# Kernel tuning notes

Hardware: AMD Instinct MI355X
Metric: run time of the kernel (lower is better)

The kernel has to match this reference:

```python
import jax, jax.numpy as jnp
import numpy as np

B, T, HW, N, HID, K, OUT = 8, 64, 64, 64, 64, 2, 1
DT = 0.1


def setup_inputs() -> dict:
    key = jax.random.key(0)
    ks = jax.random.split(key, 16)
    nrm = lambda k, shape, s: jax.random.normal(k, shape, jnp.float32) * s
    return {
        "frames": jax.random.uniform(ks[0], (B, T, HW, HW, 3), jnp.float32),
        "adjacency": jax.random.uniform(ks[1], (B, T, N, N), jnp.float32) / N,
        "hidden0": jnp.zeros((B, N, HID), jnp.float32),
        "Wc1": nrm(ks[2], (32, 3, 3, 3), 0.3), "bc1": jnp.zeros(32, jnp.float32),
        "Wc2": nrm(ks[3], (64, 32, 3, 3), 0.08), "bc2": jnp.zeros(64, jnp.float32),
        "Wc3": nrm(ks[4], (128, 64, 3, 3), 0.06), "bc3": jnp.zeros(128, jnp.float32),
        "We": nrm(ks[5], (128, HID), 0.09), "be": jnp.zeros(HID, jnp.float32),
        "Wh": nrm(ks[6], (K + 1, HID, HID), 0.12),
        "Wx": nrm(ks[7], (K + 1, HID, HID), 0.12),
        "bg": jnp.zeros(HID, jnp.float32),
        "tau": jnp.ones(HID, jnp.float32),
        "Ap": nrm(ks[8], (HID,), 1.0),
        "Wd1": nrm(ks[9], (HID, 128), 0.12), "bd1": jnp.zeros(128, jnp.float32),
        "Wd2": nrm(ks[10], (128, 64), 0.09), "bd2": jnp.zeros(64, jnp.float32),
        "Wd3": nrm(ks[11], (64, OUT), 0.12), "bd3": jnp.zeros(OUT, jnp.float32),
    }


def _conv_relu(x, w, b, stride):
    # torch Conv2d(k=3, stride=2, padding=1) == explicit padding (1,1)
    y = jax.lax.conv_general_dilated(
        x, w, (stride, stride), [(1, 1), (1, 1)],
        dimension_numbers=("NCHW", "OIHW", "NCHW"))
    return jax.nn.relu(y + b[None, :, None, None])


def _forward(frames, adjacency, hidden0, Wc1, bc1, Wc2, bc2, Wc3, bc3,
             We, be, Wh, Wx, bg, tau, Ap, Wd1, bd1, Wd2, bd2, Wd3, bd3):
    Bn, Tn, Hh, Ww, C = frames.shape
    # faithful to torch .view(-1, C, H, W): raw memory reinterpretation
    x = frames.reshape(Bn * Tn, C, Hh, Ww)
    x = _conv_relu(x, Wc1, bc1, 2)   # [BT,32,32,32]
    x = _conv_relu(x, Wc2, bc2, 2)   # [BT,64,16,16]
    x = _conv_relu(x, Wc3, bc3, 2)   # [BT,128,8,8]; AdaptiveAvgPool2d((8,8)) is identity here
    feats = x.reshape(Bn, Tn, 128, 8, 8).transpose(0, 1, 3, 4, 2).reshape(Bn, Tn, 64, 128)
    node = feats @ We + be           # [B,T,N,HID]

    Kp = Wh.shape[0] - 1
    eye = jnp.eye(adjacency.shape[-1], dtype=frames.dtype)

    def step(h, inputs):
        xt, At = inputs              # [B,N,HID], [B,N,N]
        powers = [jnp.broadcast_to(eye, At.shape)]
        p = At
        for _ in range(Kp):          # static K-loop -> [I, A, ..., A^K]
            powers.append(p)
            p = jnp.matmul(p, At)
        S = jnp.stack(powers)        # [K+1,B,N,N]
        z = jnp.einsum("bnd,kde->kbne", h, Wh) + jnp.einsum("bnd,kde->kbne", xt, Wx)
        gc = jnp.einsum("kbnm,kbme->bne", S, z) + bg
        f = jnp.tanh(gc)
        h_next = h + DT * (-(1.0 / tau + f) * h + f * Ap)  # liquid time-constant Euler step
        m = h_next.mean(axis=1)      # [B,HID]
        d = jax.nn.relu(m @ Wd1 + bd1)
        d = jax.nn.relu(d @ Wd2 + bd2)
        c = d @ Wd3 + bd3            # [B,OUT]
        return h_next, c

    xs = (node.transpose(1, 0, 2, 3), adjacency.transpose(1, 0, 2, 3))
    final_h, controls = jax.lax.scan(step, hidden0, xs)
    controls = controls.transpose(1, 0, 2)  # [B,T,OUT]
    return controls, final_h


def reference(frames, adjacency, hidden0, Wc1, bc1, Wc2, bc2, Wc3, bc3,
              We, be, Wh, Wx, bg, tau, Ap, Wd1, bd1, Wd2, bd2, Wd3, bd3):
    return _forward(frames, adjacency, hidden0, Wc1, bc1, Wc2, bc2, Wc3, bc3,
                    We, be, Wh, Wx, bg, tau, Ap, Wd1, bd1, Wd2, bd2, Wd3, bd3)
```

## Files before the change

### kernel.cpp

```cpp
#include <hip/hip_runtime.h>
#include <hip/hip_bf16.h>

#define SH 68
#define DT_C 0.1f

typedef short bfrag __attribute__((ext_vector_type(8)));
typedef _Float16 hfrag __attribute__((ext_vector_type(8)));
typedef float f32x4 __attribute__((ext_vector_type(4)));

union FU { bfrag v; unsigned short s[8]; uint4 q; };
union HU { hfrag v; unsigned short s[8]; uint4 q; };

__device__ __forceinline__ unsigned short bf16_rn(float x) {
  union { float f; unsigned u; } v; v.f = x;
  unsigned r = v.u + 0x7fffu + ((v.u >> 16) & 1u);
  return (unsigned short)(r >> 16);
}
__device__ __forceinline__ float bf16_tof(unsigned short h) {
  union { unsigned u; float f; } v; v.u = ((unsigned)h) << 16; return v.f;
}
__device__ __forceinline__ unsigned short bfu(float x) {
  union { __hip_bfloat16 b; unsigned short u; } cv;
  cv.b = __float2bfloat16(x);
  return cv.u;
}
__device__ __forceinline__ float tanh_f(float x) {
  return 1.0f - 2.0f / (__expf(2.0f * x) + 1.0f);
}
__device__ __forceinline__ void h16split(float v, unsigned short& hu, unsigned short& lu) {
  union { _Float16 h; unsigned short u; } a, b;
  a.h = (_Float16)v;
  b.h = (_Float16)(v - (float)a.h);
  hu = a.u; lu = b.u;
}
__device__ __forceinline__ unsigned short h16hi(float v) {
  union { _Float16 h; unsigned short u; } a; a.h = (_Float16)v; return a.u;
}

__device__ __forceinline__ void mm16(const float* __restrict__ A,
                                     const float* __restrict__ B, int sb,
                                     float acc[4][4], int n0, int e0) {
  #pragma unroll 4
  for (int k4 = 0; k4 < 16; ++k4) {
    float4 av0 = *(const float4*)(A + (n0+0)*SH + k4*4);
    float4 av1 = *(const float4*)(A + (n0+1)*SH + k4*4);
    float4 av2 = *(const float4*)(A + (n0+2)*SH + k4*4);
    float4 av3 = *(const float4*)(A + (n0+3)*SH + k4*4);
    const float a0j[4] = {av0.x, av0.y, av0.z, av0.w};
    const float a1j[4] = {av1.x, av1.y, av1.z, av1.w};
    const float a2j[4] = {av2.x, av2.y, av2.z, av2.w};
    const float a3j[4] = {av3.x, av3.y, av3.z, av3.w};
    #pragma unroll
    for (int j = 0; j < 4; ++j) {
      const float4 bv = *(const float4*)(B + (k4*4+j)*sb + e0);
      acc[0][0]+=a0j[j]*bv.x; acc[0][1]+=a0j[j]*bv.y; acc[0][2]+=a0j[j]*bv.z; acc[0][3]+=a0j[j]*bv.w;
      acc[1][0]+=a1j[j]*bv.x; acc[1][1]+=a1j[j]*bv.y; acc[1][2]+=a1j[j]*bv.z; acc[1][3]+=a1j[j]*bv.w;
      acc[2][0]+=a2j[j]*bv.x; acc[2][1]+=a2j[j]*bv.y; acc[2][2]+=a2j[j]*bv.z; acc[2][3]+=a2j[j]*bv.w;
      acc[3][0]+=a3j[j]*bv.x; acc[3][1]+=a3j[j]*bv.y; acc[3][2]+=a3j[j]*bv.z; acc[3][3]+=a3j[j]*bv.w;
    }
  }
}

__global__ __launch_bounds__(256) void wprep_k(const float* __restrict__ Wc2,
                                               const float* __restrict__ Wc3,
                                               const float* __restrict__ Wh,
                                               const float* __restrict__ We,
                                               unsigned short* __restrict__ W2h,
                                               unsigned short* __restrict__ W2l,
                                               unsigned short* __restrict__ W3h,
                                               unsigned short* __restrict__ W3l,
                                               unsigned short* __restrict__ WTh,
                                               unsigned short* __restrict__ WTl,
                                               unsigned short* __restrict__ WeTh,
                                               unsigned short* __restrict__ WeTl) {
  int i = blockIdx.x * 256 + threadIdx.x;
  if (i < 18432) {
    int oc = i / 288, rem = i % 288, pos = rem >> 5, ic = rem & 31;
    float v = Wc2[oc*288 + ic*9 + pos];
    h16split(v, W2h[i], W2l[i]);
  } else if (i < 18432 + 73728) {
    int j = i - 18432;
    int oc = j / 576, rem = j % 576, pos = rem >> 6, ic = rem & 63;
    float v = Wc3[oc*576 + ic*9 + pos];
    h16split(v, W3h[j], W3l[j]);
  } else if (i < 18432 + 73728 + 12288) {
    int j = i - 92160;
    int k3 = j >> 12, rem = j & 4095, din = rem >> 6, dout = rem & 63;
    float v = Wh[j];
    unsigned short hi = bf16_rn(v);
    WTh[k3*4096 + dout*64 + din] = hi;
    WTl[k3*4096 + dout*64 + din] = bf16_rn(v - bf16_tof(hi));
  } else if (i < 18432 + 73728 + 12288 + 8192) {
    int j = i - 104448;
    int e = j >> 7, oc = j & 127;
    float v = We[oc*64 + e];
    h16split(v, WeTh[j], WeTl[j]);
  }
}

__global__ __launch_bounds__(256) void conv1_k(const float* __restrict__ frames,
                                               const float* __restrict__ W,
                                               const float* __restrict__ bias,
                                               unsigned short* __restrict__ c1h) {
  __shared__ __align__(16) float sIn[12288];
  int bt = blockIdx.x, tid = threadIdx.x;
  const float4* src = (const float4*)(frames + (size_t)bt * 12288);
  for (int i = tid; i < 3072; i += 256) ((float4*)sIn)[i] = src[i];
  __syncthreads();
  for (int p = tid; p < 1024; p += 256) {
    int ho = p >> 5, wo = p & 31, hi0 = ho*2-1, wi0 = wo*2-1;
    int obase = (((ho*2 + (wo&1))*16 + (wo>>1)))*8;
    for (int ocb = 0; ocb < 4; ++ocb) {
      float acc[8];
      #pragma unroll
      for (int j = 0; j < 8; ++j) acc[j] = bias[ocb*8+j];
      for (int ic = 0; ic < 3; ++ic) {
        float win[9];
        #pragma unroll
        for (int kh = 0; kh < 3; ++kh) {
          int hi = hi0 + kh;
          #pragma unroll
          for (int kw = 0; kw < 3; ++kw) {
            int wi = wi0 + kw;
            win[kh*3+kw] = (hi>=0 && hi<64 && wi>=0 && wi<64) ? sIn[ic*4096 + hi*64 + wi] : 0.f;
          }
        }
        #pragma unroll
        for (int j = 0; j < 8; ++j) {
          const float* wp = W + (size_t)(ocb*8+j)*27 + ic*9;
          #pragma unroll
          for (int k = 0; k < 9; ++k) acc[j] += win[k] * wp[k];
        }
      }
      ushort hh[8];
      #pragma unroll
      for (int j = 0; j < 8; ++j) hh[j] = h16hi(fmaxf(acc[j], 0.f));
      *(uint4*)&c1h[(size_t)bt*32768 + ocb*8192 + obase] = *(uint4*)hh;
    }
  }
}

#define MFMAH(a, bb, cc) __builtin_amdgcn_mfma_f32_16x16x32_f16((a), (bb), (cc), 0, 0, 0)

__global__ __launch_bounds__(256) void conv2m_k(const unsigned short* __restrict__ c1h,
                                                const unsigned short* __restrict__ W2h,
                                                const unsigned short* __restrict__ W2l,
                                                const float* __restrict__ bias,
                                                unsigned short* __restrict__ c2h) {
  __shared__ __align__(16) unsigned short sH[32768];
  int bt = blockIdx.x, tid = threadIdx.x;
  {
    const uint4* gh = (const uint4*)(c1h + (size_t)bt*32768);
    for (int i = tid; i < 4096; i += 256) ((uint4*)sH)[i] = gh[i];
  }
  __syncthreads();
  int lane = tid & 63, w = tid >> 6, g = lane >> 4, c = lane & 15;
  f32x4 acc[4][4] = {};
  const uint4 z4 = make_uint4(0,0,0,0);
  #pragma unroll
  for (int pos = 0; pos < 9; ++pos) {
    const int kh = pos / 3, kw = pos % 3;
    HU Ah[4];
    #pragma unroll
    for (int m = 0; m < 4; ++m) {
      int pix = w*64 + m*16 + c;
      int ho = pix >> 4, wo = pix & 15;
      int hi = 2*ho - 1 + kh, wi = 2*wo - 1 + kw;
      bool ok = (hi >= 0) & (wi >= 0);
      int hic = ok ? hi : 0, wic = ok ? wi : 0;
      int a = (((g*32 + hic)*2 + (wic & 1))*16 + (wic >> 1))*8;
      uint4 vh = *(const uint4*)&sH[a];
      Ah[m].q = ok ? vh : z4;
    }
    HU Bh[4], Bl[4];
    #pragma unroll
    for (int n = 0; n < 4; ++n) {
      int off = (n*16 + c)*288 + pos*32 + g*8;
      Bh[n].q = *(const uint4*)(W2h + off);
      Bl[n].q = *(const uint4*)(W2l + off);
    }
    #pragma unroll
    for (int m = 0; m < 4; ++m)
      #pragma unroll
      for (int n = 0; n < 4; ++n) {
        acc[m][n] = MFMAH(Ah[m].v, Bh[n].v, acc[m][n]);
        acc[m][n] = MFMAH(Ah[m].v, Bl[n].v, acc[m][n]);
      }
  }
  #pragma unroll
  for (int n = 0; n < 4; ++n) {
    int oc = n*16 + c;
    float bv = bias[oc];
    int ks3 = oc >> 3, il = oc & 7;
    #pragma unroll
    for (int m = 0; m < 4; ++m) {
      #pragma unroll
      for (int r = 0; r < 4; ++r) {
        int pix = w*64 + m*16 + 4*g + r;
        int ho = pix >> 4, wo = pix & 15;
        float v = fmaxf(acc[m][n][r] + bv, 0.f);
        size_t dst = (size_t)bt*16384 + ((((ks3*16 + ho)*2 + (wo&1))*8 + (wo>>1)))*8 + il;
        c2h[dst] = h16hi(v);
      }
    }
  }
}

__global__ __launch_bounds__(256) void conv3e_k(const unsigned short* __restrict__ c2h,
                                                const unsigned short* __restrict__ W3h,
                                                const unsigned short* __restrict__ W3l,
                                                const float* __restrict__ bias,
                                                const unsigned short* __restrict__ WeTh,
                                                const unsigned short* __restrict__ WeTl,
                                                const float* __restrict__ be,
                                                float* __restrict__ node) {
  __shared__ __align__(16) unsigned short sH[16384];
  __shared__ __align__(16) unsigned short sF[64*136];
  int bt = blockIdx.x, tid = threadIdx.x;
  {
    const uint4* gh = (const uint4*)(c2h + (size_t)bt*16384);
    for (int i = tid; i < 2048; i += 256) ((uint4*)sH)[i] = gh[i];
  }
  __syncthreads();
  int lane = tid & 63, w = tid >> 6, g = lane >> 4, c = lane & 15;
  f32x4 acc[8] = {};
  const uint4 z4 = make_uint4(0,0,0,0);
  int pix = w*16 + c;
  int ho = pix >> 3, wo = pix & 7;
  #pragma unroll
  for (int pos = 0; pos < 9; ++pos) {
    const int kh = pos / 3, kw = pos % 3;
    int hi = 2*ho - 1 + kh, wi = 2*wo - 1 + kw;
    bool ok = (hi >= 0) & (wi >= 0);
    int hic = ok ? hi : 0, wic = ok ? wi : 0;
    #pragma unroll
    for (int ih = 0; ih < 2; ++ih) {
      int icg = ih*4 + g;
      int a = ((((icg*16 + hic)*2 + (wic & 1))*8 + (wic >> 1)))*8;
      HU Ah;
      uint4 vh = *(const uint4*)&sH[a];
      Ah.q = ok ? vh : z4;
      #pragma unroll
      for (int n = 0; n < 8; ++n) {
        int off = (n*16 + c)*576 + pos*64 + ih*32 + g*8;
        HU Bh, Bl;
        Bh.q = *(const uint4*)(W3h + off);
        Bl.q = *(const uint4*)(W3l + off);
        acc[n] = MFMAH(Ah.v, Bh.v, acc[n]);
        acc[n] = MFMAH(Ah.v, Bl.v, acc[n]);
      }
    }
  }
  #pragma unroll
  for (int n = 0; n < 8; ++n) {
    int oc = n*16 + c;
    float bv = bias[oc];
    #pragma unroll
    for (int r = 0; r < 4; ++r) {
      int po = w*16 + 4*g + r;
      sF[po*136 + oc] = h16hi(fmaxf(acc[n][r] + bv, 0.f));
    }
  }
  __syncthreads();
  f32x4 eacc[4] = {{0.f,0.f,0.f,0.f},{0.f,0.f,0.f,0.f},{0.f,0.f,0.f,0.f},{0.f,0.f,0.f,0.f}};
  #pragma unroll
  for (int kt = 0; kt < 4; ++kt) {
    HU Af;
    Af.q = *(const uint4*)&sF[(w*16 + c)*136 + kt*32 + g*8];
    #pragma unroll
    for (int n = 0; n < 4; ++n) {
      int off = (n*16 + c)*128 + kt*32 + g*8;
      HU Bh, Bl;
      Bh.q = *(const uint4*)(WeTh + off);
      Bl.q = *(const uint4*)(WeTl + off);
      eacc[n] = MFMAH(Af.v, Bh.v, eacc[n]);
      eacc[n] = MFMAH(Af.v, Bl.v, eacc[n]);
    }
  }
  #pragma unroll
  for (int n = 0; n < 4; ++n) {
    int e = n*16 + c;
    float bev = be[e];
    #pragma unroll
    for (int r = 0; r < 4; ++r) {
      int po = w*16 + 4*g + r;
      node[(size_t)bt*4096 + po*64 + e] = eacc[n][r] + bev;
    }
  }
}

__global__ __launch_bounds__(256) void prep_k(const float* __restrict__ adj,
                                              const float* __restrict__ node,
                                              const float* __restrict__ Wx,
                                              unsigned short* __restrict__ Abf,
                                              unsigned short* __restrict__ A2bf,
                                              float* __restrict__ gxg) {
  __shared__ __align__(16) float sA[64*SH], sA2[64*SH], sN[64*SH], sZ[64*SH];
  int bt = blockIdx.x, tid = threadIdx.x;
  {
    const float4* a4 = (const float4*)(adj + (size_t)bt * 4096);
    const float4* n4 = (const float4*)(node + (size_t)bt * 4096);
    for (int i = tid; i < 1024; i += 256) {
      int r = i >> 4, c = (i & 15) * 4;
      *(float4*)&sA[r*SH+c] = a4[i];
      *(float4*)&sN[r*SH+c] = n4[i];
    }
  }
  __syncthreads();
  int lane = tid & 63, w = tid >> 6, nsub = lane >> 4, eb = lane & 15;
  int n0 = w*16 + nsub*4, e0 = eb*4;
  float4* gxout = (float4*)(gxg + (size_t)bt * 4096);
  for (int i = tid; i < 1024; i += 256) {
    int r = i >> 4, c0 = (i & 15) * 4;
    ushort4 o;
    o.x = bf16_rn(sA[r*SH+c0+0]); o.y = bf16_rn(sA[r*SH+c0+1]);
    o.z = bf16_rn(sA[r*SH+c0+2]); o.w = bf16_rn(sA[r*SH+c0+3]);
    *(ushort4*)&Abf[(size_t)bt*4096 + r*64 + c0] = o;
  }
  {
    float a2t[4][4] = {};
    mm16(sA, sA, SH, a2t, n0, e0);
    #pragma unroll
    for (int jj = 0; jj < 4; ++jj) {
      *(float4*)&sA2[(n0+jj)*SH+e0] = make_float4(a2t[jj][0], a2t[jj][1], a2t[jj][2], a2t[jj][3]);
      ushort4 o;
      o.x = bf16_rn(a2t[jj][0]); o.y = bf16_rn(a2t[jj][1]);
      o.z = bf16_rn(a2t[jj][2]); o.w = bf16_rn(a2t[jj][3]);
      *(ushort4*)&A2bf[(size_t)bt*4096 + (n0+jj)*64 + e0] = o;
    }
  }
  {
    float t[4][4] = {};
    mm16(sN, Wx + 4096, 64, t, n0, e0);
    #pragma unroll
    for (int jj = 0; jj < 4; ++jj)
      *(float4*)&sZ[(n0+jj)*SH+e0] = make_float4(t[jj][0], t[jj][1], t[jj][2], t[jj][3]);
  }
  __syncthreads();
  float gx[4][4] = {};
  mm16(sA, sZ, SH, gx, n0, e0);
  __syncthreads();
  {
    float t[4][4] = {};
    mm16(sN, Wx + 8192, 64, t, n0, e0);
    #pragma unroll
    for (int jj = 0; jj < 4; ++jj)
      *(float4*)&sZ[(n0+jj)*SH+e0] = make_float4(t[jj][0], t[jj][1], t[jj][2], t[jj][3]);
  }
  __syncthreads();
  mm16(sA2, sZ, SH, gx, n0, e0);
  mm16(sN, Wx, 64, gx, n0, e0);
  #pragma unroll
  for (int jj = 0; jj < 4; ++jj)
    gxout[(n0+jj)*16 + eb] = make_float4(gx[jj][0], gx[jj][1], gx[jj][2], gx[jj][3]);
}

#define MFMA(a, bb, cc) __builtin_amdgcn_mfma_f32_16x16x32_bf16((a), (bb), (cc), 0, 0, 0)

__global__ __launch_bounds__(1024, 4) void seq2_k(
    const unsigned short* __restrict__ Abf, const unsigned short* __restrict__ A2bf,
    const float* __restrict__ gxg, const float* __restrict__ h0,
    const unsigned short* __restrict__ WTh, const unsigned short* __restrict__ WTl,
    const float* __restrict__ bg, const float* __restrict__ tau, const float* __restrict__ Apv,
    float* __restrict__ mout, float* __restrict__ out) {
  __shared__ unsigned short sHh[64*72];
  __shared__ unsigned short sA[2][64*72], sA2[2][64*72];
  __shared__ unsigned short sZ1[64*72], sZ2[64*72];
  __shared__ float sPart[64*17];
  int b = blockIdx.x, tid = threadIdx.x;
  int lane = tid & 63, w = tid >> 6, g = lane >> 4, c = lane & 15;
  int mt = w & 3, nt = w >> 2;
  int e = nt*16 + c;
  int mrow = mt*16 + 4*g;
  float itau = 1.f/tau[e], apv = Apv[e], bgv = bg[e];
  FU wf[3][2][2];
  #pragma unroll
  for (int k3 = 0; k3 < 3; ++k3)
    #pragma unroll
    for (int kt = 0; kt < 2; ++kt) {
      int off = k3*4096 + e*64 + kt*32 + 8*g;
      wf[k3][kt][0].q = *(const uint4*)(WTh + off);
      wf[k3][kt][1].q = *(const uint4*)(WTl + off);
    }
  float hm[4];
  #pragma unroll
  for (int r = 0; r < 4; ++r) hm[r] = h0[(size_t)b*4096 + (mrow+r)*64 + e];
  #pragma unroll
  for (int r = 0; r < 4; ++r) sHh[(mrow+r)*72 + e] = bfu(hm[r]);
  {
    int row = tid >> 4, k0 = (tid & 15) * 4;
    *(uint2*)&sA[0][row*72 + k0]  = *(const uint2*)(Abf  + (size_t)b*64*4096 + tid*4);
    *(uint2*)&sA2[0][row*72 + k0] = *(const uint2*)(A2bf + (size_t)b*64*4096 + tid*4);
  }
  __syncthreads();
  #pragma unroll 1
  for (int t = 0; t < 64; ++t) {
    int cur = t & 1;
    size_t bt = (size_t)b*64 + t;
    int tn = (t < 63) ? t + 1 : t;
    uint2 pa  = *(const uint2*)(Abf  + ((size_t)b*64 + tn)*4096 + tid*4);
    uint2 pa2 = *(const uint2*)(A2bf + ((size_t)b*64 + tn)*4096 + tid*4);
    float gxv[4];
    {
      const float* gp = gxg + bt*4096;
      #pragma unroll
      for (int r = 0; r < 4; ++r) gxv[r] = gp[(mrow+r)*64 + e];
    }
    FU ha[2];
    #pragma unroll
    for (int kt = 0; kt < 2; ++kt)
      ha[kt].q = *(const uint4*)&sHh[(mt*16 + c)*72 + kt*32 + 8*g];
    f32x4 a1 = {0.f,0.f,0.f,0.f}, a2 = {0.f,0.f,0.f,0.f};
    #pragma unroll
    for (int kt = 0; kt < 2; ++kt) {
      a1 = MFMA(ha[kt].v, wf[1][kt][0].v, a1);
      a1 = MFMA(ha[kt].v, wf[1][kt][1].v, a1);
      a2 = MFMA(ha[kt].v, wf[2][kt][0].v, a2);
      a2 = MFMA(ha[kt].v, wf[2][kt][1].v, a2);
    }
    {
      ushort4 o1, o2;
      o1.x = bfu(a1[0]); o1.y = bfu(a1[1]); o1.z = bfu(a1[2]); o1.w = bfu(a1[3]);
      o2.x = bfu(a2[0]); o2.y = bfu(a2[1]); o2.z = bfu(a2[2]); o2.w = bfu(a2[3]);
      *(ushort4*)&sZ1[e*72 + mrow] = o1;
      *(ushort4*)&sZ2[e*72 + mrow] = o2;
    }
    __syncthreads();
    f32x4 acc = {0.f,0.f,0.f,0.f};
    #pragma unroll
    for (int kt = 0; kt < 2; ++kt) {
      FU aA, aA2, z1f, z2f;
      int ao = (mt*16 + c)*72 + kt*32 + 8*g;
      aA.q  = *(const uint4*)&sA[cur][ao];
      aA2.q = *(const uint4*)&sA2[cur][ao];
      z1f.q = *(const uint4*)&sZ1[e*72 + kt*32 + 8*g];
      z2f.q = *(const uint4*)&sZ2[e*72 + kt*32 + 8*g];
      acc = MFMA(ha[kt].v, wf[0][kt][0].v, acc);
      acc = MFMA(ha[kt].v, wf[0][kt][1].v, acc);
      acc = MFMA(aA.v,  z1f.v, acc);
      acc = MFMA(aA2.v, z2f.v, acc);
    }
    float ps = 0.f;
    #pragma unroll
    for (int r = 0; r < 4; ++r) {
      float gc = acc[r] + gxv[r] + bgv;
      float f = tanh_f(gc);
      float hn = hm[r] + DT_C * (-(itau + f) * hm[r] + f * apv);
      hm[r] = hn;
      ps += hn;
      sHh[(mrow+r)*72 + e] = bfu(hn);
    }
    sPart[e*17 + mt*4 + g] = ps;
    {
      int row = tid >> 4, k0 = (tid & 15) * 4;
      *(uint2*)&sA[cur^1][row*72 + k0]  = pa;
      *(uint2*)&sA2[cur^1][row*72 + k0] = pa2;
    }
    __syncthreads();
    if (lane < 4) {
      int ee = w*4 + lane;
      float s = 0.f;
      #pragma unroll
      for (int j = 0; j < 16; ++j) s += sPart[ee*17 + j];
      mout[bt*64 + ee] = s * (1.0f / 64.0f);
    }
  }
  #pragma unroll
  for (int r = 0; r < 4; ++r)
    out[512 + (size_t)b*4096 + (mrow+r)*64 + e] = hm[r];
}

__global__ __launch_bounds__(128) void dec_k(const float* __restrict__ mout,
                                             const float* __restrict__ Wd1, const float* __restrict__ bd1,
                                             const float* __restrict__ Wd2, const float* __restrict__ bd2,
                                             const float* __restrict__ Wd3, const float* __restrict__ bd3,
                                             float* __restrict__ out) {
  __shared__ float sm[64], sd1[128], sd2[64];
  int bt = blockIdx.x, tid = threadIdx.x;
  if (tid < 64) sm[tid] = mout[(size_t)bt*64 + tid];
  __syncthreads();
  {
    float a = bd1[tid];
    #pragma unroll 8
    for (int e = 0; e < 64; ++e) a += sm[e] * Wd1[e*128 + tid];
    sd1[tid] = fmaxf(a, 0.f);
  }
  __syncthreads();
  if (tid < 64) {
    float a = bd2[tid];
    #pragma unroll 8
    for (int i = 0; i < 128; ++i) a += sd1[i] * Wd2[i*64 + tid];
    sd2[tid] = fmaxf(a, 0.f);
  }
  __syncthreads();
  if (tid < 64) {
    float p = sd2[tid] * Wd3[tid];
    #pragma unroll
    for (int off = 32; off > 0; off >>= 1) p += __shfl_down(p, off, 64);
    if (tid == 0) out[bt] = p + bd3[0];
  }
}

extern "C" void kernel_launch(void* const* d_in, const int* in_sizes, int n_in,
                              void* d_out, int out_size, void* d_ws, size_t ws_size,
                              hipStream_t stream) {
  const float* frames = (const float*)d_in[0];
  const float* adj    = (const float*)d_in[1];
  const float* h0     = (const float*)d_in[2];
  const float* Wc1 = (const float*)d_in[3];  const float* bc1 = (const float*)d_in[4];
  const float* Wc2 = (const float*)d_in[5];  const float* bc2 = (const float*)d_in[6];
  const float* Wc3 = (const float*)d_in[7];  const float* bc3 = (const float*)d_in[8];
  const float* We  = (const float*)d_in[9];  const float* be  = (const float*)d_in[10];
  const float* Wh  = (const float*)d_in[11]; const float* Wx  = (const float*)d_in[12];
  const float* bg  = (const float*)d_in[13]; const float* tau = (const float*)d_in[14];
  const float* Ap  = (const float*)d_in[15];
  const float* Wd1 = (const float*)d_in[16]; const float* bd1 = (const float*)d_in[17];
  const float* Wd2 = (const float*)d_in[18]; const float* bd2 = (const float*)d_in[19];
  const float* Wd3 = (const float*)d_in[20]; const float* bd3 = (const float*)d_in[21];

  float* ws = (float*)d_ws;
  unsigned short* c1h = (unsigned short*)(ws);
  unsigned short* c2h = (unsigned short*)(ws + 16777216);
  unsigned short* W2h = (unsigned short*)(ws + 20971520);
  unsigned short* W2l = (unsigned short*)(ws + 20980736);
  unsigned short* W3h = (unsigned short*)(ws + 20989952);
  unsigned short* W3l = (unsigned short*)(ws + 21026816);
  unsigned short* WTh = (unsigned short*)(ws + 21063680);
  unsigned short* WTl = (unsigned short*)(ws + 21069824);
  unsigned short* WeTh = (unsigned short*)(ws + 21075968);
  unsigned short* WeTl = (unsigned short*)(ws + 21080064);
  float* node = ws + 4194304;
  float* gx   = ws + 6291456;
  unsigned short* Abf  = (unsigned short*)(ws + 8388608);
  unsigned short* A2bf = (unsigned short*)(ws + 9437184);
  float* mo   = ws + 10485760;
  float* out  = (float*)d_out;

  wprep_k <<<440, 256, 0, stream>>>(Wc2, Wc3, Wh, We, W2h, W2l, W3h, W3l, WTh, WTl, WeTh, WeTl);
  conv1_k <<<512, 256, 0, stream>>>(frames, Wc1, bc1, c1h);
  conv2m_k<<<512, 256, 0, stream>>>(c1h, W2h, W2l, bc2, c2h);
  conv3e_k<<<512, 256, 0, stream>>>(c2h, W3h, W3l, bc3, WeTh, WeTl, be, node);
  prep_k  <<<512, 256, 0, stream>>>(adj, node, Wx, Abf, A2bf, gx);
  seq2_k  <<<8,  1024, 0, stream>>>(Abf, A2bf, gx, h0, WTh, WTl, bg, tau, Ap, mo, out);
  dec_k   <<<512, 128, 0, stream>>>(mo, Wd1, bd1, Wd2, bd2, Wd3, bd3, out);
}
```

Measured before the change: 302.2 us.

## Fuse conv1, conv2, conv3, embedding and graph prep into one per-frame kernel

```diff
diff --git a/kernel.cpp b/kernel.cpp
--- a/kernel.cpp
+++ b/kernel.cpp
@@ -37,26 +37,18 @@
   union { _Float16 h; unsigned short u; } a; a.h = (_Float16)v; return a.u;
 }
 
-__device__ __forceinline__ void mm16(const float* __restrict__ A,
-                                     const float* __restrict__ B, int sb,
-                                     float acc[4][4], int n0, int e0) {
+__device__ __forceinline__ void mm1x4(const float* __restrict__ A,
+                                      const float* __restrict__ B, int sb,
+                                      float acc[4], int n, int e0) {
   #pragma unroll 4
   for (int k4 = 0; k4 < 16; ++k4) {
-    float4 av0 = *(const float4*)(A + (n0+0)*SH + k4*4);
-    float4 av1 = *(const float4*)(A + (n0+1)*SH + k4*4);
-    float4 av2 = *(const float4*)(A + (n0+2)*SH + k4*4);
-    float4 av3 = *(const float4*)(A + (n0+3)*SH + k4*4);
-    const float a0j[4] = {av0.x, av0.y, av0.z, av0.w};
-    const float a1j[4] = {av1.x, av1.y, av1.z, av1.w};
-    const float a2j[4] = {av2.x, av2.y, av2.z, av2.w};
-    const float a3j[4] = {av3.x, av3.y, av3.z, av3.w};
+    float4 av = *(const float4*)(A + n*SH + k4*4);
+    const float aj[4] = {av.x, av.y, av.z, av.w};
     #pragma unroll
     for (int j = 0; j < 4; ++j) {
       const float4 bv = *(const float4*)(B + (k4*4+j)*sb + e0);
-      acc[0][0]+=a0j[j]*bv.x; acc[0][1]+=a0j[j]*bv.y; acc[0][2]+=a0j[j]*bv.z; acc[0][3]+=a0j[j]*bv.w;
-      acc[1][0]+=a1j[j]*bv.x; acc[1][1]+=a1j[j]*bv.y; acc[1][2]+=a1j[j]*bv.z; acc[1][3]+=a1j[j]*bv.w;
-      acc[2][0]+=a2j[j]*bv.x; acc[2][1]+=a2j[j]*bv.y; acc[2][2]+=a2j[j]*bv.z; acc[2][3]+=a2j[j]*bv.w;
-      acc[3][0]+=a3j[j]*bv.x; acc[3][1]+=a3j[j]*bv.y; acc[3][2]+=a3j[j]*bv.z; acc[3][3]+=a3j[j]*bv.w;
+      acc[0] += aj[j]*bv.x; acc[1] += aj[j]*bv.y;
+      acc[2] += aj[j]*bv.z; acc[3] += aj[j]*bv.w;
     }
   }
 }
@@ -98,261 +90,206 @@
   }
 }
 
-__global__ __launch_bounds__(256) void conv1_k(const float* __restrict__ frames,
-                                               const float* __restrict__ W,
-                                               const float* __restrict__ bias,
-                                               unsigned short* __restrict__ c1h) {
-  __shared__ __align__(16) float sIn[12288];
+#define MFMAH(a, bb, cc) __builtin_amdgcn_mfma_f32_16x16x32_f16((a), (bb), (cc), 0, 0, 0)
+
+__global__ __launch_bounds__(1024, 4) void mega_k(
+    const float* __restrict__ frames, const float* __restrict__ Wc1, const float* __restrict__ bc1,
+    const unsigned short* __restrict__ W2h, const unsigned short* __restrict__ W2l,
+    const float* __restrict__ bc2,
+    const unsigned short* __restrict__ W3h, const unsigned short* __restrict__ W3l,
+    const float* __restrict__ bc3,
+    const unsigned short* __restrict__ WeTh, const unsigned short* __restrict__ WeTl,
+    const float* __restrict__ be,
+    const float* __restrict__ adj, const float* __restrict__ Wx,
+    unsigned short* __restrict__ Abf, unsigned short* __restrict__ A2bf,
+    float* __restrict__ gxg) {
+  __shared__ __align__(16) unsigned char smem[119808];
+  float* sIn = (float*)smem;
+  unsigned short* sC1 = (unsigned short*)(smem + 49152);
+  unsigned short* sC2 = (unsigned short*)smem;
+  unsigned short* sF  = (unsigned short*)(smem + 32768);
+  float* sN  = (float*)(smem + 50176);
+  float* sA  = (float*)(smem + 67584);
+  float* sA2 = (float*)(smem + 84992);
+  float* sZ  = (float*)(smem + 102400);
+
   int bt = blockIdx.x, tid = threadIdx.x;
-  const float4* src = (const float4*)(frames + (size_t)bt * 12288);
-  for (int i = tid; i < 3072; i += 256) ((float4*)sIn)[i] = src[i];
-  __syncthreads();
-  for (int p = tid; p < 1024; p += 256) {
+  int lane = tid & 63, w = tid >> 6, g = lane >> 4, c = lane & 15;
+  const uint4 z4 = make_uint4(0,0,0,0);
+
+  {
+    const float4* src = (const float4*)(frames + (size_t)bt * 12288);
+    for (int i = tid; i < 3072; i += 1024) ((float4*)sIn)[i] = src[i];
+  }
+  __syncthreads();
+  {
+    int p = tid;
     int ho = p >> 5, wo = p & 31, hi0 = ho*2-1, wi0 = wo*2-1;
     int obase = (((ho*2 + (wo&1))*16 + (wo>>1)))*8;
+    float acc[32];
+    #pragma unroll
+    for (int j = 0; j < 32; ++j) acc[j] = bc1[j];
+    #pragma unroll
+    for (int ic = 0; ic < 3; ++ic) {
+      float win[9];
+      #pragma unroll
+      for (int kh = 0; kh < 3; ++kh) {
+        int hi = hi0 + kh;
+        #pragma unroll
+        for (int kw = 0; kw < 3; ++kw) {
+          int wi = wi0 + kw;
+          win[kh*3+kw] = (hi>=0 && hi<64 && wi>=0 && wi<64) ? sIn[ic*4096 + hi*64 + wi] : 0.f;
+        }
+      }
+      #pragma unroll
+      for (int j = 0; j < 32; ++j) {
+        const float* wp = Wc1 + (size_t)j*27 + ic*9;
+        #pragma unroll
+        for (int k = 0; k < 9; ++k) acc[j] += win[k] * wp[k];
+      }
+    }
+    #pragma unroll
     for (int ocb = 0; ocb < 4; ++ocb) {
-      float acc[8];
-      #pragma unroll
-      for (int j = 0; j < 8; ++j) acc[j] = bias[ocb*8+j];
-      for (int ic = 0; ic < 3; ++ic) {
-        float win[9];
-        #pragma unroll
-        for (int kh = 0; kh < 3; ++kh) {
-          int hi = hi0 + kh;
-          #pragma unroll
-          for (int kw = 0; kw < 3; ++kw) {
-            int wi = wi0 + kw;
-            win[kh*3+kw] = (hi>=0 && hi<64 && wi>=0 && wi<64) ? sIn[ic*4096 + hi*64 + wi] : 0.f;
-          }
-        }
-        #pragma unroll
-        for (int j = 0; j < 8; ++j) {
-          const float* wp = W + (size_t)(ocb*8+j)*27 + ic*9;
-          #pragma unroll
-          for (int k = 0; k < 9; ++k) acc[j] += win[k] * wp[k];
-        }
-      }
       ushort hh[8];
       #pragma unroll
-      for (int j = 0; j < 8; ++j) hh[j] = h16hi(fmaxf(acc[j], 0.f));
-      *(uint4*)&c1h[(size_t)bt*32768 + ocb*8192 + obase] = *(uint4*)hh;
-    }
-  }
-}
-
-#define MFMAH(a, bb, cc) __builtin_amdgcn_mfma_f32_16x16x32_f16((a), (bb), (cc), 0, 0, 0)
-
-__global__ __launch_bounds__(256) void conv2m_k(const unsigned short* __restrict__ c1h,
-                                                const unsigned short* __restrict__ W2h,
-                                                const unsigned short* __restrict__ W2l,
-                                                const float* __restrict__ bias,
-                                                unsigned short* __restrict__ c2h) {
-  __shared__ __align__(16) unsigned short sH[32768];
-  int bt = blockIdx.x, tid = threadIdx.x;
-  {
-    const uint4* gh = (const uint4*)(c1h + (size_t)bt*32768);
-    for (int i = tid; i < 4096; i += 256) ((uint4*)sH)[i] = gh[i];
-  }
-  __syncthreads();
-  int lane = tid & 63, w = tid >> 6, g = lane >> 4, c = lane & 15;
-  f32x4 acc[4][4] = {};
-  const uint4 z4 = make_uint4(0,0,0,0);
-  #pragma unroll
-  for (int pos = 0; pos < 9; ++pos) {
-    const int kh = pos / 3, kw = pos % 3;
-    HU Ah[4];
-    #pragma unroll
-    for (int m = 0; m < 4; ++m) {
-      int pix = w*64 + m*16 + c;
-      int ho = pix >> 4, wo = pix & 15;
+      for (int j = 0; j < 8; ++j) hh[j] = h16hi(fmaxf(acc[ocb*8+j], 0.f));
+      *(uint4*)&sC1[ocb*8192 + obase] = *(uint4*)hh;
+    }
+  }
+  __syncthreads();
+  {
+    f32x4 acc2[4] = {};
+    #pragma unroll
+    for (int pos = 0; pos < 9; ++pos) {
+      const int kh = pos / 3, kw = pos % 3;
+      int hi = 2*w - 1 + kh, wi = 2*c - 1 + kw;
+      bool ok = (hi >= 0) & (wi >= 0);
+      int hic = ok ? hi : 0, wic = ok ? wi : 0;
+      int a = (((g*32 + hic)*2 + (wic & 1))*16 + (wic >> 1))*8;
+      HU Ah;
+      uint4 vh = *(const uint4*)&sC1[a];
+      Ah.q = ok ? vh : z4;
+      #pragma unroll
+      for (int n = 0; n < 4; ++n) {
+        int off = (n*16 + c)*288 + pos*32 + g*8;
+        HU Bh, Bl;
+        Bh.q = *(const uint4*)(W2h + off);
+        Bl.q = *(const uint4*)(W2l + off);
+        acc2[n] = MFMAH(Ah.v, Bh.v, acc2[n]);
+        acc2[n] = MFMAH(Ah.v, Bl.v, acc2[n]);
+      }
+    }
+    __syncthreads();
+    #pragma unroll
+    for (int n = 0; n < 4; ++n) {
+      int oc = n*16 + c;
+      float bv = bc2[oc];
+      int ks3 = oc >> 3, il = oc & 7;
+      #pragma unroll
+      for (int r = 0; r < 4; ++r) {
+        int wo2 = 4*g + r;
+        float v = fmaxf(acc2[n][r] + bv, 0.f);
+        int dst = ((((ks3*16 + w)*2 + (wo2&1))*8 + (wo2>>1)))*8 + il;
+        sC2[dst] = h16hi(v);
+      }
+    }
+  }
+  __syncthreads();
+  {
+    int mq = w & 3, nq = w >> 2;
+    int pix = mq*16 + c, ho = pix >> 3, wo = pix & 7;
+    f32x4 acc3[2] = {};
+    #pragma unroll
+    for (int pos = 0; pos < 9; ++pos) {
+      const int kh = pos / 3, kw = pos % 3;
       int hi = 2*ho - 1 + kh, wi = 2*wo - 1 + kw;
       bool ok = (hi >= 0) & (wi >= 0);
       int hic = ok ? hi : 0, wic = ok ? wi : 0;
-      int a = (((g*32 + hic)*2 + (wic & 1))*16 + (wic >> 1))*8;
-      uint4 vh = *(const uint4*)&sH[a];
-      Ah[m].q = ok ? vh : z4;
-    }
-    HU Bh[4], Bl[4];
-    #pragma unroll
-    for (int n = 0; n < 4; ++n) {
-      int off = (n*16 + c)*288 + pos*32 + g*8;
-      Bh[n].q = *(const uint4*)(W2h + off);
-      Bl[n].q = *(const uint4*)(W2l + off);
-    }
-    #pragma unroll
-    for (int m = 0; m < 4; ++m)
-      #pragma unroll
-      for (int n = 0; n < 4; ++n) {
-        acc[m][n] = MFMAH(Ah[m].v, Bh[n].v, acc[m][n]);
-        acc[m][n] = MFMAH(Ah[m].v, Bl[n].v, acc[m][n]);
-      }
-  }
-  #pragma unroll
-  for (int n = 0; n < 4; ++n) {
-    int oc = n*16 + c;
-    float bv = bias[oc];
-    int ks3 = oc >> 3, il = oc & 7;
-    #pragma unroll
-    for (int m = 0; m < 4; ++m) {
+      #pragma unroll
+      for (int ih = 0; ih < 2; ++ih) {
+        int icg = ih*4 + g;
+        int a = ((((icg*16 + hic)*2 + (wic & 1))*8 + (wic >> 1)))*8;
+        HU Ah;
+        uint4 vh = *(const uint4*)&sC2[a];
+        Ah.q = ok ? vh : z4;
+        #pragma unroll
+        for (int j = 0; j < 2; ++j) {
+          int off = ((nq*2+j)*16 + c)*576 + pos*64 + ih*32 + g*8;
+          HU Bh, Bl;
+          Bh.q = *(const uint4*)(W3h + off);
+          Bl.q = *(const uint4*)(W3l + off);
+          acc3[j] = MFMAH(Ah.v, Bh.v, acc3[j]);
+          acc3[j] = MFMAH(Ah.v, Bl.v, acc3[j]);
+        }
+      }
+    }
+    #pragma unroll
+    for (int j = 0; j < 2; ++j) {
+      int oc = (nq*2+j)*16 + c;
+      float bv = bc3[oc];
       #pragma unroll
       for (int r = 0; r < 4; ++r) {
-        int pix = w*64 + m*16 + 4*g + r;
-        int ho = pix >> 4, wo = pix & 15;
-        float v = fmaxf(acc[m][n][r] + bv, 0.f);
-        size_t dst = (size_t)bt*16384 + ((((ks3*16 + ho)*2 + (wo&1))*8 + (wo>>1)))*8 + il;
-        c2h[dst] = h16hi(v);
-      }
-    }
-  }
-}
-
-__global__ __launch_bounds__(256) void conv3e_k(const unsigned short* __restrict__ c2h,
-                                                const unsigned short* __restrict__ W3h,
-                                                const unsigned short* __restrict__ W3l,
-                                                const float* __restrict__ bias,
-                                                const unsigned short* __restrict__ WeTh,
-                                                const unsigned short* __restrict__ WeTl,
-                                                const float* __restrict__ be,
-                                                float* __restrict__ node) {
-  __shared__ __align__(16) unsigned short sH[16384];
-  __shared__ __align__(16) unsigned short sF[64*136];
-  int bt = blockIdx.x, tid = threadIdx.x;
-  {
-    const uint4* gh = (const uint4*)(c2h + (size_t)bt*16384);
-    for (int i = tid; i < 2048; i += 256) ((uint4*)sH)[i] = gh[i];
-  }
-  __syncthreads();
-  int lane = tid & 63, w = tid >> 6, g = lane >> 4, c = lane & 15;
-  f32x4 acc[8] = {};
-  const uint4 z4 = make_uint4(0,0,0,0);
-  int pix = w*16 + c;
-  int ho = pix >> 3, wo = pix & 7;
-  #pragma unroll
-  for (int pos = 0; pos < 9; ++pos) {
-    const int kh = pos / 3, kw = pos % 3;
-    int hi = 2*ho - 1 + kh, wi = 2*wo - 1 + kw;
-    bool ok = (hi >= 0) & (wi >= 0);
-    int hic = ok ? hi : 0, wic = ok ? wi : 0;
-    #pragma unroll
-    for (int ih = 0; ih < 2; ++ih) {
-      int icg = ih*4 + g;
-      int a = ((((icg*16 + hic)*2 + (wic & 1))*8 + (wic >> 1)))*8;
-      HU Ah;
-      uint4 vh = *(const uint4*)&sH[a];
-      Ah.q = ok ? vh : z4;
-      #pragma unroll
-      for (int n = 0; n < 8; ++n) {
-        int off = (n*16 + c)*576 + pos*64 + ih*32 + g*8;
-        HU Bh, Bl;
-        Bh.q = *(const uint4*)(W3h + off);
-        Bl.q = *(const uint4*)(W3l + off);
-        acc[n] = MFMAH(Ah.v, Bh.v, acc[n]);
-        acc[n] = MFMAH(Ah.v, Bl.v, acc[n]);
-      }
-    }
-  }
-  #pragma unroll
-  for (int n = 0; n < 8; ++n) {
-    int oc = n*16 + c;
-    float bv = bias[oc];
-    #pragma unroll
-    for (int r = 0; r < 4; ++r) {
-      int po = w*16 + 4*g + r;
-      sF[po*136 + oc] = h16hi(fmaxf(acc[n][r] + bv, 0.f));
-    }
-  }
-  __syncthreads();
-  f32x4 eacc[4] = {{0.f,0.f,0.f,0.f},{0.f,0.f,0.f,0.f},{0.f,0.f,0.f,0.f},{0.f,0.f,0.f,0.f}};
-  #pragma unroll
-  for (int kt = 0; kt < 4; ++kt) {
-    HU Af;
-    Af.q = *(const uint4*)&sF[(w*16 + c)*136 + kt*32 + g*8];
-    #pragma unroll
-    for (int n = 0; n < 4; ++n) {
-      int off = (n*16 + c)*128 + kt*32 + g*8;
+        int po = mq*16 + 4*g + r;
+        sF[po*136 + oc] = h16hi(fmaxf(acc3[j][r] + bv, 0.f));
+      }
+    }
+  }
+  __syncthreads();
+  {
+    int mq = w & 3, nq = w >> 2;
+    f32x4 eacc = {0.f,0.f,0.f,0.f};
+    #pragma unroll
+    for (int kt = 0; kt < 4; ++kt) {
+      HU Af;
+      Af.q = *(const uint4*)&sF[(mq*16 + c)*136 + kt*32 + g*8];
+      int off = (nq*16 + c)*128 + kt*32 + g*8;
       HU Bh, Bl;
       Bh.q = *(const uint4*)(WeTh + off);
       Bl.q = *(const uint4*)(WeTl + off);
-      eacc[n] = MFMAH(Af.v, Bh.v, eacc[n]);
-      eacc[n] = MFMAH(Af.v, Bl.v, eacc[n]);
-    }
-  }
-  #pragma unroll
-  for (int n = 0; n < 4; ++n) {
-    int e = n*16 + c;
+      eacc = MFMAH(Af.v, Bh.v, eacc);
+      eacc = MFMAH(Af.v, Bl.v, eacc);
+    }
+    int e = nq*16 + c;
     float bev = be[e];
     #pragma unroll
     for (int r = 0; r < 4; ++r) {
-      int po = w*16 + 4*g + r;
-      node[(size_t)bt*4096 + po*64 + e] = eacc[n][r] + bev;
-    }
-  }
-}
-
-__global__ __launch_bounds__(256) void prep_k(const float* __restrict__ adj,
-                                              const float* __restrict__ node,
-                                              const float* __restrict__ Wx,
-                                              unsigned short* __restrict__ Abf,
-                                              unsigned short* __restrict__ A2bf,
-                                              float* __restrict__ gxg) {
-  __shared__ __align__(16) float sA[64*SH], sA2[64*SH], sN[64*SH], sZ[64*SH];
-  int bt = blockIdx.x, tid = threadIdx.x;
-  {
-    const float4* a4 = (const float4*)(adj + (size_t)bt * 4096);
-    const float4* n4 = (const float4*)(node + (size_t)bt * 4096);
-    for (int i = tid; i < 1024; i += 256) {
-      int r = i >> 4, c = (i & 15) * 4;
-      *(float4*)&sA[r*SH+c] = a4[i];
-      *(float4*)&sN[r*SH+c] = n4[i];
-    }
-  }
-  __syncthreads();
-  int lane = tid & 63, w = tid >> 6, nsub = lane >> 4, eb = lane & 15;
-  int n0 = w*16 + nsub*4, e0 = eb*4;
-  float4* gxout = (float4*)(gxg + (size_t)bt * 4096);
-  for (int i = tid; i < 1024; i += 256) {
-    int r = i >> 4, c0 = (i & 15) * 4;
+      int po = mq*16 + 4*g + r;
+      sN[po*68 + e] = eacc[r] + bev;
+    }
+    float4 av = ((const float4*)(adj + (size_t)bt * 4096))[tid];
+    int rr = tid >> 4, cc = (tid & 15) * 4;
+    *(float4*)&sA[rr*68 + cc] = av;
     ushort4 o;
-    o.x = bf16_rn(sA[r*SH+c0+0]); o.y = bf16_rn(sA[r*SH+c0+1]);
-    o.z = bf16_rn(sA[r*SH+c0+2]); o.w = bf16_rn(sA[r*SH+c0+3]);
-    *(ushort4*)&Abf[(size_t)bt*4096 + r*64 + c0] = o;
-  }
-  {
-    float a2t[4][4] = {};
-    mm16(sA, sA, SH, a2t, n0, e0);
-    #pragma unroll
-    for (int jj = 0; jj < 4; ++jj) {
-      *(float4*)&sA2[(n0+jj)*SH+e0] = make_float4(a2t[jj][0], a2t[jj][1], a2t[jj][2], a2t[jj][3]);
-      ushort4 o;
-      o.x = bf16_rn(a2t[jj][0]); o.y = bf16_rn(a2t[jj][1]);
-      o.z = bf16_rn(a2t[jj][2]); o.w = bf16_rn(a2t[jj][3]);
-      *(ushort4*)&A2bf[(size_t)bt*4096 + (n0+jj)*64 + e0] = o;
-    }
-  }
-  {
-    float t[4][4] = {};
-    mm16(sN, Wx + 4096, 64, t, n0, e0);
-    #pragma unroll
-    for (int jj = 0; jj < 4; ++jj)
-      *(float4*)&sZ[(n0+jj)*SH+e0] = make_float4(t[jj][0], t[jj][1], t[jj][2], t[jj][3]);
-  }
-  __syncthreads();
-  float gx[4][4] = {};
-  mm16(sA, sZ, SH, gx, n0, e0);
-  __syncthreads();
-  {
-    float t[4][4] = {};
-    mm16(sN, Wx + 8192, 64, t, n0, e0);
-    #pragma unroll
-    for (int jj = 0; jj < 4; ++jj)
-      *(float4*)&sZ[(n0+jj)*SH+e0] = make_float4(t[jj][0], t[jj][1], t[jj][2], t[jj][3]);
-  }
-  __syncthreads();
-  mm16(sA2, sZ, SH, gx, n0, e0);
-  mm16(sN, Wx, 64, gx, n0, e0);
-  #pragma unroll
-  for (int jj = 0; jj < 4; ++jj)
-    gxout[(n0+jj)*16 + eb] = make_float4(gx[jj][0], gx[jj][1], gx[jj][2], gx[jj][3]);
+    o.x = bf16_rn(av.x); o.y = bf16_rn(av.y); o.z = bf16_rn(av.z); o.w = bf16_rn(av.w);
+    *(ushort4*)&Abf[(size_t)bt*4096 + rr*64 + cc] = o;
+  }
+  __syncthreads();
+  int n = tid >> 4, e0 = (tid & 15) * 4;
+  {
+    float a2acc[4] = {0.f,0.f,0.f,0.f};
+    mm1x4(sA, sA, 68, a2acc, n, e0);
+    *(float4*)&sA2[n*68 + e0] = make_float4(a2acc[0], a2acc[1], a2acc[2], a2acc[3]);
+    ushort4 o;
+    o.x = bf16_rn(a2acc[0]); o.y = bf16_rn(a2acc[1]);
+    o.z = bf16_rn(a2acc[2]); o.w = bf16_rn(a2acc[3]);
+    *(ushort4*)&A2bf[(size_t)bt*4096 + n*64 + e0] = o;
+    float z1acc[4] = {0.f,0.f,0.f,0.f};
+    mm1x4(sN, Wx + 4096, 64, z1acc, n, e0);
+    *(float4*)&sZ[n*68 + e0] = make_float4(z1acc[0], z1acc[1], z1acc[2], z1acc[3]);
+  }
+  __syncthreads();
+  float gxa[4] = {0.f,0.f,0.f,0.f};
+  mm1x4(sA, sZ, 68, gxa, n, e0);
+  __syncthreads();
+  {
+    float z2acc[4] = {0.f,0.f,0.f,0.f};
+    mm1x4(sN, Wx + 8192, 64, z2acc, n, e0);
+    *(float4*)&sZ[n*68 + e0] = make_float4(z2acc[0], z2acc[1], z2acc[2], z2acc[3]);
+  }
+  __syncthreads();
+  mm1x4(sA2, sZ, 68, gxa, n, e0);
+  mm1x4(sN, Wx, 64, gxa, n, e0);
+  *(float4*)(gxg + (size_t)bt*4096 + n*64 + e0) = make_float4(gxa[0], gxa[1], gxa[2], gxa[3]);
 }
 
 #define MFMA(a, bb, cc) __builtin_amdgcn_mfma_f32_16x16x32_bf16((a), (bb), (cc), 0, 0, 0)
@@ -519,8 +456,6 @@
   const float* Wd3 = (const float*)d_in[20]; const float* bd3 = (const float*)d_in[21];
 
   float* ws = (float*)d_ws;
-  unsigned short* c1h = (unsigned short*)(ws);
-  unsigned short* c2h = (unsigned short*)(ws + 16777216);
   unsigned short* W2h = (unsigned short*)(ws + 20971520);
   unsigned short* W2l = (unsigned short*)(ws + 20980736);
   unsigned short* W3h = (unsigned short*)(ws + 20989952);
@@ -529,18 +464,15 @@
   unsigned short* WTl = (unsigned short*)(ws + 21069824);
   unsigned short* WeTh = (unsigned short*)(ws + 21075968);
   unsigned short* WeTl = (unsigned short*)(ws + 21080064);
-  float* node = ws + 4194304;
   float* gx   = ws + 6291456;
   unsigned short* Abf  = (unsigned short*)(ws + 8388608);
   unsigned short* A2bf = (unsigned short*)(ws + 9437184);
   float* mo   = ws + 10485760;
   float* out  = (float*)d_out;
 
-  wprep_k <<<440, 256, 0, stream>>>(Wc2, Wc3, Wh, We, W2h, W2l, W3h, W3l, WTh, WTl, WeTh, WeTl);
-  conv1_k <<<512, 256, 0, stream>>>(frames, Wc1, bc1, c1h);
-  conv2m_k<<<512, 256, 0, stream>>>(c1h, W2h, W2l, bc2, c2h);
-  conv3e_k<<<512, 256, 0, stream>>>(c2h, W3h, W3l, bc3, WeTh, WeTl, be, node);
-  prep_k  <<<512, 256, 0, stream>>>(adj, node, Wx, Abf, A2bf, gx);
-  seq2_k  <<<8,  1024, 0, stream>>>(Abf, A2bf, gx, h0, WTh, WTl, bg, tau, Ap, mo, out);
-  dec_k   <<<512, 128, 0, stream>>>(mo, Wd1, bd1, Wd2, bd2, Wd3, bd3, out);
-}
+  wprep_k<<<440, 256, 0, stream>>>(Wc2, Wc3, Wh, We, W2h, W2l, W3h, W3l, WTh, WTl, WeTh, WeTl);
+  mega_k <<<512, 1024, 0, stream>>>(frames, Wc1, bc1, W2h, W2l, bc2, W3h, W3l, bc3,
+                                    WeTh, WeTl, be, adj, Wx, Abf, A2bf, gx);
+  seq2_k <<<8,  1024, 0, stream>>>(Abf, A2bf, gx, h0, WTh, WTl, bg, tau, Ap, mo, out);
+  dec_k  <<<512, 128, 0, stream>>>(mo, Wd1, bd1, Wd2, bd2, Wd3, bd3, out);
+}
```

Result: slower. 339.5 us (+12.3%).
